# Kernel optimization log

Hardware: AMD Instinct MI355X
Metric: run time of the kernel (lower is better)

## Reference

```python
import jax, jax.numpy as jnp
import numpy as np


def ternarize_weight(w):
    # abs-mean threshold quantization to {-am, 0, +am}
    abs_mean = jnp.maximum(jnp.abs(w).mean(), 1e-5)
    thr = 0.7 * abs_mean
    q = jnp.where(w > thr, 1.0, jnp.where(w < -thr, -1.0, 0.0))
    # STE: forward value is q*abs_mean, grad flows to w as identity
    return w + jax.lax.stop_gradient(q * abs_mean - w)


def rotate_half(x):
    x1, x2 = jnp.split(x, 2, axis=-1)
    return jnp.concatenate([-x2, x1], axis=-1)


def setup_inputs() -> dict:
    key = jax.random.key(0)
    k1, k2, k3, k4, k5 = jax.random.split(key, 5)
    B, T, C, H = 2, 2048, 1024, 16
    D = C // H
    x = jax.random.normal(k1, (B, T, C), dtype=jnp.float32)
    cos = jax.random.uniform(k2, (1, 1, T, D), dtype=jnp.float32)
    sin = jax.random.uniform(k3, (1, 1, T, D), dtype=jnp.float32)
    w_qkv = jax.random.normal(k4, (3 * C, C), dtype=jnp.float32) / np.sqrt(C)
    w_proj = jax.random.normal(k5, (C, C), dtype=jnp.float32) / np.sqrt(C)
    return {"x": x, "cos": cos, "sin": sin, "w_qkv": w_qkv, "w_proj": w_proj}


def reference(x, cos, sin, w_qkv, w_proj):
    B, T, C = x.shape
    H = 16
    D = C // H
    wq = ternarize_weight(w_qkv)
    wp = ternarize_weight(w_proj)
    qkv = x @ wq.T  # [B,T,3C]
    q, k, v = jnp.split(qkv, 3, axis=-1)
    # [B,T,C] -> [B,H,T,D]
    q = q.reshape(B, T, H, D).transpose(0, 2, 1, 3)
    k = k.reshape(B, T, H, D).transpose(0, 2, 1, 3)
    v = v.reshape(B, T, H, D).transpose(0, 2, 1, 3)
    # RoPE
    q = q * cos + rotate_half(q) * sin
    k = k * cos + rotate_half(k) * sin
    # causal SDPA
    scale = 1.0 / np.sqrt(D)
    scores = jnp.einsum("bhqd,bhkd->bhqk", q, k) * scale
    causal = jnp.tril(jnp.ones((T, T), dtype=bool))
    scores = jnp.where(causal, scores, jnp.finfo(scores.dtype).min)
    attn = jax.nn.softmax(scores, axis=-1)
    y = jnp.einsum("bhqk,bhkd->bhqd", attn, v)  # [B,H,T,D]
    y = y.transpose(0, 2, 1, 3).reshape(B, T, C)
    return y @ wp.T
```

## Files before the change

kernel.cpp:

```cpp
#include <hip/hip_runtime.h>
#include <hip/hip_bf16.h>

#define B_ 2
#define T_ 2048
#define C_ 1024
#define H_ 16
#define D_ 64
#define M_ 4096
#define N3C 3072

using short8  = __attribute__((ext_vector_type(8))) short;
using floatx4 = __attribute__((ext_vector_type(4))) float;
typedef unsigned int u32;

__device__ __forceinline__ unsigned short f2b(float f) {
  __hip_bfloat16 h = __float2bfloat16(f);
  return *reinterpret_cast<unsigned short*>(&h);
}
__device__ __forceinline__ float b2f(unsigned short u) {
  union { unsigned int i; float f; } x; x.i = ((unsigned int)u) << 16; return x.f;
}

__device__ __forceinline__ void gll16(const void* g, void* l) {
  __builtin_amdgcn_global_load_lds((const __attribute__((address_space(1))) u32*)g,
                                   (__attribute__((address_space(3))) u32*)l, 16, 0, 0);
}


__global__ void zero_sums(double* sums) {
  if (threadIdx.x < 2) sums[threadIdx.x] = 0.0;
}

__global__ void abs_sum2(const float* __restrict__ wq, const float* __restrict__ wp,
                         double* __restrict__ sums) {
  __shared__ double red[4];
  const float* w = blockIdx.y ? wp : wq;
  const int n4 = blockIdx.y ? (C_ * C_ / 4) : (3 * C_ * C_ / 4);
  int stride = gridDim.x * blockDim.x;
  double s = 0.0;
  for (int i = blockIdx.x * blockDim.x + threadIdx.x; i < n4; i += stride) {
    float4 v = ((const float4*)w)[i];
    s += (double)fabsf(v.x) + (double)fabsf(v.y) + (double)fabsf(v.z) + (double)fabsf(v.w);
  }
  #pragma unroll
  for (int off = 32; off > 0; off >>= 1)
    s += __shfl_down(s, off, 64);
  if ((threadIdx.x & 63) == 0) red[threadIdx.x >> 6] = s;
  __syncthreads();
  if (threadIdx.x == 0) atomicAdd(sums + blockIdx.y, (red[0] + red[1]) + (red[2] + red[3]));
}

__global__ void ternarize_all(const float* __restrict__ wq, const float* __restrict__ wp,
                              unsigned short* __restrict__ oq, unsigned short* __restrict__ op,
                              const double* __restrict__ sums, float* __restrict__ ams) {
  const int NQ = 3 * C_ * C_;
  const int NP = C_ * C_;
  int i = blockIdx.x * blockDim.x + threadIdx.x;
  float am0 = fmaxf((float)(sums[0] * (1.0 / NQ)), 1e-5f);
  float am1 = fmaxf((float)(sums[1] * (1.0 / NP)), 1e-5f);
  if (i == 0) { ams[0] = am0; ams[1] = am1; }
  if (i < NQ) {
    float thr = 0.7f * am0, x = wq[i];
    oq[i] = (x > thr) ? 0x3F80u : ((x < -thr) ? 0xBF80u : 0u);
  } else if (i < NQ + NP) {
    int j = i - NQ;
    float thr = 0.7f * am1, x = wp[j];
    op[j] = (x > thr) ? 0x3F80u : ((x < -thr) ? 0xBF80u : 0u);
  }
}

__global__ void cvt_f32_bf16(const float* __restrict__ in, unsigned short* __restrict__ out, int n4) {
  int i = blockIdx.x * blockDim.x + threadIdx.x;
  if (i < n4) {
    float4 v = ((const float4*)in)[i];
    ushort4 o; o.x = f2b(v.x); o.y = f2b(v.y); o.z = f2b(v.z); o.w = f2b(v.w);
    ((ushort4*)out)[i] = o;
  }
}


__global__ __launch_bounds__(256) void gemm_qkv(const unsigned short* __restrict__ A,
                                                const unsigned short* __restrict__ W,
                                                const float* __restrict__ scale_ptr,
                                                const float* __restrict__ cosp,
                                                const float* __restrict__ sinp,
                                                unsigned short* __restrict__ Qb,
                                                unsigned short* __restrict__ Kb,
                                                unsigned short* __restrict__ Vb) {
  const int K = C_;
  __shared__ __attribute__((aligned(16))) unsigned short As[128 * 32];
  __shared__ __attribute__((aligned(16))) unsigned short Ws[128 * 32];
  const int tid = threadIdx.x, lane = tid & 63, wv = tid >> 6;
  const int m = lane & 15, g = lane >> 4;
  const int m0 = blockIdx.y * 128, n0 = blockIdx.x * 128;
  const int wm = (wv >> 1) * 64, wn = (wv & 1) * 64;

  const int srow = wv * 16 + (lane >> 2);
  const int skoff = (lane & 3) * 8;
  const unsigned short* ga0 = A + (size_t)(m0 + srow) * K + skoff;
  const unsigned short* ga1 = A + (size_t)(m0 + 64 + srow) * K + skoff;
  const unsigned short* gw0 = W + (size_t)(n0 + srow) * K + skoff;
  const unsigned short* gw1 = W + (size_t)(n0 + 64 + srow) * K + skoff;
  unsigned short* la0 = As + (wv * 16) * 32;
  unsigned short* la1 = As + (64 + wv * 16) * 32;
  unsigned short* lw0 = Ws + (wv * 16) * 32;
  unsigned short* lw1 = Ws + (64 + wv * 16) * 32;

  floatx4 acc[4][4] = {};
  for (int kc = 0; kc < K; kc += 32) {
    __syncthreads();
    gll16(ga0, la0); gll16(ga1, la1); gll16(gw0, lw0); gll16(gw1, lw1);
    ga0 += 32; ga1 += 32; gw0 += 32; gw1 += 32;
    __syncthreads();
    short8 af[4], wf[4];
    #pragma unroll
    for (int r = 0; r < 4; r++)
      af[r] = *(const short8*)&As[(wm + r * 16 + m) * 32 + g * 8];
    #pragma unroll
    for (int c = 0; c < 4; c++)
      wf[c] = *(const short8*)&Ws[(wn + c * 16 + m) * 32 + g * 8];
    #pragma unroll
    for (int r = 0; r < 4; r++)
      #pragma unroll
      for (int c = 0; c < 4; c++)
        acc[r][c] = __builtin_amdgcn_mfma_f32_16x16x32_bf16(af[r], wf[c], acc[r][c], 0, 0, 0);
  }

  const float am = *scale_ptr;
  const int sect = n0 >> 10;
  const int nloc = n0 & 1023;
  const int h = (nloc + wn) >> 6;
  if (sect < 2) {
    unsigned short* dst = sect ? Kb : Qb;
    const float sc = sect ? am : am * 0.18033688011112042f;
    #pragma unroll
    for (int r = 0; r < 4; r++)
      #pragma unroll
      for (int i = 0; i < 4; i++) {
        int row = m0 + wm + r * 16 + g * 4 + i;
        int t = row & (T_ - 1), b = row >> 11;
        size_t obase = ((size_t)(b * H_ + h) * T_ + t) * 64;
        #pragma unroll
        for (int c = 0; c < 4; c++) {
          int p = c * 16 + m;
          float cv = cosp[t * 64 + p], sv = sinp[t * 64 + p];
          float a = acc[r][c][i], pt = acc[r][c ^ 2][i];
          float val = (c < 2) ? (a * cv - pt * sv) : (a * cv + pt * sv);
          dst[obase + p] = f2b(val * sc);
        }
      }
  } else {
    #pragma unroll
    for (int r = 0; r < 4; r++)
      #pragma unroll
      for (int i = 0; i < 4; i++) {
        int row = m0 + wm + r * 16 + g * 4 + i;
        int t = row & (T_ - 1), b = row >> 11;
        size_t obase = ((size_t)(b * H_ + h) * T_ + t) * 64;
        #pragma unroll
        for (int c = 0; c < 4; c++)
          Vb[obase + c * 16 + m] = f2b(acc[r][c][i] * am);
      }
  }
}


__global__ __launch_bounds__(256) void gemm128(const unsigned short* __restrict__ A,
                                               const unsigned short* __restrict__ W,
                                               const float* __restrict__ scale_ptr,
                                               float* __restrict__ Cout,
                                               int N, int K) {
  __shared__ __attribute__((aligned(16))) unsigned short As[128 * 32];
  __shared__ __attribute__((aligned(16))) unsigned short Ws[128 * 32];
  const int tid = threadIdx.x, lane = tid & 63, wv = tid >> 6;
  const int m = lane & 15, g = lane >> 4;
  const int m0 = blockIdx.y * 128, n0 = blockIdx.x * 128;
  const int wm = (wv >> 1) * 64, wn = (wv & 1) * 64;

  const int srow = wv * 16 + (lane >> 2);
  const int skoff = (lane & 3) * 8;
  const unsigned short* ga0 = A + (size_t)(m0 + srow) * K + skoff;
  const unsigned short* ga1 = A + (size_t)(m0 + 64 + srow) * K + skoff;
  const unsigned short* gw0 = W + (size_t)(n0 + srow) * K + skoff;
  const unsigned short* gw1 = W + (size_t)(n0 + 64 + srow) * K + skoff;
  unsigned short* la0 = As + (wv * 16) * 32;
  unsigned short* la1 = As + (64 + wv * 16) * 32;
  unsigned short* lw0 = Ws + (wv * 16) * 32;
  unsigned short* lw1 = Ws + (64 + wv * 16) * 32;

  floatx4 acc[4][4] = {};
  for (int kc = 0; kc < K; kc += 32) {
    __syncthreads();
    gll16(ga0, la0); gll16(ga1, la1); gll16(gw0, lw0); gll16(gw1, lw1);
    ga0 += 32; ga1 += 32; gw0 += 32; gw1 += 32;
    __syncthreads();
    short8 af[4], wf[4];
    #pragma unroll
    for (int r = 0; r < 4; r++)
      af[r] = *(const short8*)&As[(wm + r * 16 + m) * 32 + g * 8];
    #pragma unroll
    for (int c = 0; c < 4; c++)
      wf[c] = *(const short8*)&Ws[(wn + c * 16 + m) * 32 + g * 8];
    #pragma unroll
    for (int r = 0; r < 4; r++)
      #pragma unroll
      for (int c = 0; c < 4; c++)
        acc[r][c] = __builtin_amdgcn_mfma_f32_16x16x32_bf16(af[r], wf[c], acc[r][c], 0, 0, 0);
  }

  const float scale = *scale_ptr;
  #pragma unroll
  for (int r = 0; r < 4; r++)
    #pragma unroll
    for (int c = 0; c < 4; c++)
      #pragma unroll
      for (int i = 0; i < 4; i++) {
        int row = m0 + wm + r * 16 + g * 4 + i;
        int col = n0 + wn + c * 16 + m;
        Cout[(size_t)row * N + col] = acc[r][c][i] * scale;
      }
}


__global__ __launch_bounds__(256) void v_transpose(const unsigned short* __restrict__ Vb,
                                                   unsigned short* __restrict__ Vtb) {
  __shared__ unsigned short L[64][65];
  const int bh = blockIdx.y, t0 = blockIdx.x * 64;
  const size_t hb = (size_t)bh * T_ * 64;
  #pragma unroll
  for (int it = 0; it < 16; it++) {
    int idx = it * 256 + threadIdx.x;
    int tl = idx >> 6, d = idx & 63;
    L[tl][d] = Vb[hb + (size_t)(t0 + tl) * 64 + d];
  }
  __syncthreads();
  #pragma unroll
  for (int it = 0; it < 16; it++) {
    int idx = it * 256 + threadIdx.x;
    int dr = idx >> 6, tl = idx & 63;
    Vtb[hb + (size_t)dr * T_ + t0 + tl] = L[tl][dr];
  }
}


__global__ __launch_bounds__(256) void flash_mfma(const unsigned short* __restrict__ Qb,
                                                  const unsigned short* __restrict__ Kb,
                                                  const unsigned short* __restrict__ Vtb,
                                                  unsigned short* __restrict__ Y) {
  __shared__ __align__(16) unsigned short Ktile[2][64][64];
  __shared__ __align__(16) unsigned short Vtile[2][64][64];
  __shared__ __align__(16) unsigned short Plds[4][16][72];
  const int lane = threadIdx.x & 63;
  const int wv = threadIdx.x >> 6;
  const int m = lane & 15, g = lane >> 4;
  const int gid = blockIdx.x;
  const int xcd = gid & 7, j = gid >> 3;
  const int bh = xcd * 4 + (j >> 4);
  const int pr = j & 15;
  const int b = bh >> 4, h = bh & 15;
  const size_t hb = (size_t)bh * T_ * 64;
  const unsigned short* Kbh = Kb + hb;
  const unsigned short* Vbh = Vtb + hb;
  const int r8 = lane >> 3, cc8 = lane & 7;
  const int gcol = ((cc8 ^ r8) << 3);

  #pragma unroll
  for (int sp = 0; sp < 2; sp++) {
    const int s = sp ? pr : (31 - pr);
    const int qbase = s * 64 + wv * 16;
    const int q_glob = qbase + m;
    const int ntiles = s + 1;

    const unsigned short* qp = Qb + hb + (size_t)(qbase + m) * 64 + g * 8;
    short8 qf0 = *(const short8*)qp;
    short8 qf1 = *(const short8*)(qp + 32);

    floatx4 O[4] = {};
    float lsum = 0.f;

    if (sp) __syncthreads();
    #pragma unroll
    for (int cc = 0; cc < 2; cc++) {
      int row = wv * 16 + cc * 8;
      gll16(Kbh + (size_t)(row + r8) * 64 + gcol, &Ktile[0][row][0]);
      gll16(Vbh + (size_t)(row + r8) * T_ + gcol, &Vtile[0][row][0]);
    }

    for (int kt = 0; kt < ntiles; kt++) {
      const int buf = kt & 1;
      const int kb = kt * 64;
      __syncthreads();
      if (kt + 1 < ntiles) {
        const int kb2 = kb + 64;
        #pragma unroll
        for (int cc = 0; cc < 2; cc++) {
          int row = wv * 16 + cc * 8;
          gll16(Kbh + (size_t)(kb2 + row + r8) * 64 + gcol, &Ktile[1 - buf][row][0]);
          gll16(Vbh + (size_t)(row + r8) * T_ + kb2 + gcol, &Vtile[1 - buf][row][0]);
        }
      }
      floatx4 S[4];
      #pragma unroll
      for (int mt = 0; mt < 4; mt++) {
        int row = mt * 16 + m;
        short8 kf0 = *(const short8*)&Ktile[buf][row][(g ^ (m & 7)) << 3];
        short8 kf1 = *(const short8*)&Ktile[buf][row][((g + 4) ^ (m & 7)) << 3];
        floatx4 sv = {};
        sv = __builtin_amdgcn_mfma_f32_16x16x32_bf16(kf0, qf0, sv, 0, 0, 0);
        sv = __builtin_amdgcn_mfma_f32_16x16x32_bf16(kf1, qf1, sv, 0, 0, 0);
        S[mt] = sv;
      }
      if (kt + 1 < ntiles) {
        #pragma unroll
        for (int mt = 0; mt < 4; mt++) {
          float e0 = exp2f(S[mt][0]), e1 = exp2f(S[mt][1]);
          float e2 = exp2f(S[mt][2]), e3 = exp2f(S[mt][3]);
          lsum += (e0 + e1) + (e2 + e3);
          ushort4 o; o.x = f2b(e0); o.y = f2b(e1); o.z = f2b(e2); o.w = f2b(e3);
          *(ushort4*)&Plds[wv][m][mt * 16 + g * 4] = o;
        }
      } else {
        #pragma unroll
        for (int mt = 0; mt < 4; mt++) {
          float e[4];
          #pragma unroll
          for (int r = 0; r < 4; r++) {
            int kg = kb + mt * 16 + g * 4 + r;
            e[r] = (kg <= q_glob) ? exp2f(S[mt][r]) : 0.f;
          }
          lsum += (e[0] + e[1]) + (e[2] + e[3]);
          ushort4 o; o.x = f2b(e[0]); o.y = f2b(e[1]); o.z = f2b(e[2]); o.w = f2b(e[3]);
          *(ushort4*)&Plds[wv][m][mt * 16 + g * 4] = o;
        }
      }
      short8 pa0 = *(const short8*)&Plds[wv][m][g * 8];
      short8 pa1 = *(const short8*)&Plds[wv][m][32 + g * 8];
      #pragma unroll
      for (int nt = 0; nt < 4; nt++) {
        int row = nt * 16 + m;
        short8 v0 = *(const short8*)&Vtile[buf][row][(g ^ (m & 7)) << 3];
        short8 v1 = *(const short8*)&Vtile[buf][row][((g + 4) ^ (m & 7)) << 3];
        O[nt] = __builtin_amdgcn_mfma_f32_16x16x32_bf16(pa0, v0, O[nt], 0, 0, 0);
        O[nt] = __builtin_amdgcn_mfma_f32_16x16x32_bf16(pa1, v1, O[nt], 0, 0, 0);
      }
    }

    lsum += __shfl_xor(lsum, 16, 64);
    lsum += __shfl_xor(lsum, 32, 64);
    float li[4];
    #pragma unroll
    for (int r = 0; r < 4; r++) li[r] = 1.0f / __shfl(lsum, g * 4 + r, 64);
    #pragma unroll
    for (int nt = 0; nt < 4; nt++)
      #pragma unroll
      for (int r = 0; r < 4; r++) {
        int trow = qbase + g * 4 + r;
        int col = h * 64 + nt * 16 + m;
        Y[(size_t)(b * T_ + trow) * C_ + col] = f2b(O[nt][r] * li[r]);
      }
  }
}


extern "C" void kernel_launch(void* const* d_in, const int* in_sizes, int n_in,
                              void* d_out, int out_size, void* d_ws, size_t ws_size,
                              hipStream_t stream) {
  (void)in_sizes; (void)n_in; (void)out_size; (void)ws_size;
  const float* x      = (const float*)d_in[0];
  const float* cosp   = (const float*)d_in[1];
  const float* sinp   = (const float*)d_in[2];
  const float* w_qkv  = (const float*)d_in[3];
  const float* w_proj = (const float*)d_in[4];
  float* out = (float*)d_out;

  char* ws = (char*)d_ws;
  double* sums = (double*)ws;
  float*  ams  = (float*)(ws + 16);
  unsigned short* wqkv_b  = (unsigned short*)(ws + 256);
  unsigned short* wproj_b = wqkv_b + (size_t)N3C * C_;
  unsigned short* xb      = wproj_b + (size_t)C_ * C_;
  unsigned short* Qb      = xb + (size_t)M_ * C_;
  unsigned short* Kb      = Qb + (size_t)B_ * H_ * T_ * D_;
  unsigned short* Vb      = Kb + (size_t)B_ * H_ * T_ * D_;
  unsigned short* Vtb     = Vb + (size_t)B_ * H_ * T_ * D_;
  unsigned short* yb      = Vtb + (size_t)B_ * H_ * T_ * D_;

  zero_sums<<<1, 64, 0, stream>>>(sums);
  abs_sum2<<<dim3(256, 2), 256, 0, stream>>>(w_qkv, w_proj, sums);
  ternarize_all<<<(4 * C_ * C_) / 256, 256, 0, stream>>>(w_qkv, w_proj, wqkv_b, wproj_b,
                                                         sums, ams);
  cvt_f32_bf16<<<(M_ * C_ / 4 + 255) / 256, 256, 0, stream>>>(x, xb, M_ * C_ / 4);
  gemm_qkv<<<dim3(N3C / 128, M_ / 128), 256, 0, stream>>>(xb, wqkv_b, ams + 0,
                                                          cosp, sinp, Qb, Kb, Vb);
  v_transpose<<<dim3(T_ / 64, B_ * H_), 256, 0, stream>>>(Vb, Vtb);
  flash_mfma<<<512, 256, 0, stream>>>(Qb, Kb, Vtb, yb);
  gemm128<<<dim3(C_ / 128, M_ / 128), 256, 0, stream>>>(yb, wproj_b, ams + 1, out, C_, C_);
}
```

Before: 225.5 us.

## Fuse weight/activation conversion, write V transposed, widen flash query tiles

```diff
diff --git a/kernel.cpp b/kernel.cpp
--- a/kernel.cpp
+++ b/kernel.cpp
@@ -26,10 +26,6 @@
                                    (__attribute__((address_space(3))) u32*)l, 16, 0, 0);
 }
 
-
-__global__ void zero_sums(double* sums) {
-  if (threadIdx.x < 2) sums[threadIdx.x] = 0.0;
-}
 
 __global__ void abs_sum2(const float* __restrict__ wq, const float* __restrict__ wp,
                          double* __restrict__ sums) {
@@ -50,9 +46,11 @@
   if (threadIdx.x == 0) atomicAdd(sums + blockIdx.y, (red[0] + red[1]) + (red[2] + red[3]));
 }
 
-__global__ void ternarize_all(const float* __restrict__ wq, const float* __restrict__ wp,
-                              unsigned short* __restrict__ oq, unsigned short* __restrict__ op,
-                              const double* __restrict__ sums, float* __restrict__ ams) {
+__global__ void tern_cvt(const float* __restrict__ wq, const float* __restrict__ wp,
+                         const float* __restrict__ x,
+                         unsigned short* __restrict__ oq, unsigned short* __restrict__ op,
+                         unsigned short* __restrict__ xb,
+                         const double* __restrict__ sums, float* __restrict__ ams) {
   const int NQ = 3 * C_ * C_;
   const int NP = C_ * C_;
   int i = blockIdx.x * blockDim.x + threadIdx.x;
@@ -60,21 +58,17 @@
   float am1 = fmaxf((float)(sums[1] * (1.0 / NP)), 1e-5f);
   if (i == 0) { ams[0] = am0; ams[1] = am1; }
   if (i < NQ) {
-    float thr = 0.7f * am0, x = wq[i];
-    oq[i] = (x > thr) ? 0x3F80u : ((x < -thr) ? 0xBF80u : 0u);
+    float thr = 0.7f * am0, v = wq[i];
+    oq[i] = (v > thr) ? 0x3F80u : ((v < -thr) ? 0xBF80u : 0u);
   } else if (i < NQ + NP) {
     int j = i - NQ;
-    float thr = 0.7f * am1, x = wp[j];
-    op[j] = (x > thr) ? 0x3F80u : ((x < -thr) ? 0xBF80u : 0u);
-  }
-}
-
-__global__ void cvt_f32_bf16(const float* __restrict__ in, unsigned short* __restrict__ out, int n4) {
-  int i = blockIdx.x * blockDim.x + threadIdx.x;
-  if (i < n4) {
-    float4 v = ((const float4*)in)[i];
+    float thr = 0.7f * am1, v = wp[j];
+    op[j] = (v > thr) ? 0x3F80u : ((v < -thr) ? 0xBF80u : 0u);
+  } else {
+    int j = i - NQ - NP;
+    float4 v = ((const float4*)x)[j];
     ushort4 o; o.x = f2b(v.x); o.y = f2b(v.y); o.z = f2b(v.z); o.w = f2b(v.w);
-    ((ushort4*)out)[i] = o;
+    ((ushort4*)xb)[j] = o;
   }
 }
 
@@ -86,7 +80,7 @@
                                                 const float* __restrict__ sinp,
                                                 unsigned short* __restrict__ Qb,
                                                 unsigned short* __restrict__ Kb,
-                                                unsigned short* __restrict__ Vb) {
+                                                unsigned short* __restrict__ Vtb) {
   const int K = C_;
   __shared__ __attribute__((aligned(16))) unsigned short As[128 * 32];
   __shared__ __attribute__((aligned(16))) unsigned short Ws[128 * 32];
@@ -156,10 +150,10 @@
       for (int i = 0; i < 4; i++) {
         int row = m0 + wm + r * 16 + g * 4 + i;
         int t = row & (T_ - 1), b = row >> 11;
-        size_t obase = ((size_t)(b * H_ + h) * T_ + t) * 64;
+        size_t hbase = (size_t)(b * H_ + h) * 64 * T_;
         #pragma unroll
         for (int c = 0; c < 4; c++)
-          Vb[obase + c * 16 + m] = f2b(acc[r][c][i] * am);
+          Vtb[hbase + (size_t)(c * 16 + m) * T_ + t] = f2b(acc[r][c][i] * am);
       }
   }
 }
@@ -219,27 +213,6 @@
         int col = n0 + wn + c * 16 + m;
         Cout[(size_t)row * N + col] = acc[r][c][i] * scale;
       }
-}
-
-
-__global__ __launch_bounds__(256) void v_transpose(const unsigned short* __restrict__ Vb,
-                                                   unsigned short* __restrict__ Vtb) {
-  __shared__ unsigned short L[64][65];
-  const int bh = blockIdx.y, t0 = blockIdx.x * 64;
-  const size_t hb = (size_t)bh * T_ * 64;
-  #pragma unroll
-  for (int it = 0; it < 16; it++) {
-    int idx = it * 256 + threadIdx.x;
-    int tl = idx >> 6, d = idx & 63;
-    L[tl][d] = Vb[hb + (size_t)(t0 + tl) * 64 + d];
-  }
-  __syncthreads();
-  #pragma unroll
-  for (int it = 0; it < 16; it++) {
-    int idx = it * 256 + threadIdx.x;
-    int dr = idx >> 6, tl = idx & 63;
-    Vtb[hb + (size_t)dr * T_ + t0 + tl] = L[tl][dr];
-  }
 }
 
 
@@ -255,8 +228,8 @@
   const int m = lane & 15, g = lane >> 4;
   const int gid = blockIdx.x;
   const int xcd = gid & 7, j = gid >> 3;
-  const int bh = xcd * 4 + (j >> 4);
-  const int pr = j & 15;
+  const int bh = xcd * 4 + (j & 3);
+  const int s = 15 - (j >> 2);
   const int b = bh >> 4, h = bh & 15;
   const size_t hb = (size_t)bh * T_ * 64;
   const unsigned short* Kbh = Kb + hb;
@@ -264,41 +237,43 @@
   const int r8 = lane >> 3, cc8 = lane & 7;
   const int gcol = ((cc8 ^ r8) << 3);
 
+  const int ntiles = 2 * s + 2;
+  const int qb0 = s * 128 + wv * 32;
+  const int qb1 = qb0 + 16;
+
+  const unsigned short* qp0 = Qb + hb + (size_t)(qb0 + m) * 64 + g * 8;
+  short8 qf00 = *(const short8*)qp0;
+  short8 qf01 = *(const short8*)(qp0 + 32);
+  const unsigned short* qp1 = qp0 + 16 * 64;
+  short8 qf10 = *(const short8*)qp1;
+  short8 qf11 = *(const short8*)(qp1 + 32);
+
+  floatx4 O0[4] = {}, O1[4] = {};
+  float ls0 = 0.f, ls1 = 0.f;
+
   #pragma unroll
-  for (int sp = 0; sp < 2; sp++) {
-    const int s = sp ? pr : (31 - pr);
-    const int qbase = s * 64 + wv * 16;
-    const int q_glob = qbase + m;
-    const int ntiles = s + 1;
-
-    const unsigned short* qp = Qb + hb + (size_t)(qbase + m) * 64 + g * 8;
-    short8 qf0 = *(const short8*)qp;
-    short8 qf1 = *(const short8*)(qp + 32);
-
-    floatx4 O[4] = {};
-    float lsum = 0.f;
-
-    if (sp) __syncthreads();
-    #pragma unroll
-    for (int cc = 0; cc < 2; cc++) {
-      int row = wv * 16 + cc * 8;
-      gll16(Kbh + (size_t)(row + r8) * 64 + gcol, &Ktile[0][row][0]);
-      gll16(Vbh + (size_t)(row + r8) * T_ + gcol, &Vtile[0][row][0]);
+  for (int cc = 0; cc < 2; cc++) {
+    int row = wv * 16 + cc * 8;
+    gll16(Kbh + (size_t)(row + r8) * 64 + gcol, &Ktile[0][row][0]);
+    gll16(Vbh + (size_t)(row + r8) * T_ + gcol, &Vtile[0][row][0]);
+  }
+
+  for (int kt = 0; kt < ntiles; kt++) {
+    const int buf = kt & 1;
+    const int kb = kt * 64;
+    __syncthreads();
+    if (kt + 1 < ntiles) {
+      const int kb2 = kb + 64;
+      #pragma unroll
+      for (int cc = 0; cc < 2; cc++) {
+        int row = wv * 16 + cc * 8;
+        gll16(Kbh + (size_t)(kb2 + row + r8) * 64 + gcol, &Ktile[1 - buf][row][0]);
+        gll16(Vbh + (size_t)(row + r8) * T_ + kb2 + gcol, &Vtile[1 - buf][row][0]);
+      }
     }
-
-    for (int kt = 0; kt < ntiles; kt++) {
-      const int buf = kt & 1;
-      const int kb = kt * 64;
-      __syncthreads();
-      if (kt + 1 < ntiles) {
-        const int kb2 = kb + 64;
-        #pragma unroll
-        for (int cc = 0; cc < 2; cc++) {
-          int row = wv * 16 + cc * 8;
-          gll16(Kbh + (size_t)(kb2 + row + r8) * 64 + gcol, &Ktile[1 - buf][row][0]);
-          gll16(Vbh + (size_t)(row + r8) * T_ + kb2 + gcol, &Vtile[1 - buf][row][0]);
-        }
-      }
+    if (kb > qb0 + 31) continue;
+
+    auto do_qset = [&](short8 qa, short8 qb_, int qbase, float& lsum, floatx4* O) {
       floatx4 S[4];
       #pragma unroll
       for (int mt = 0; mt < 4; mt++) {
@@ -306,11 +281,11 @@
         short8 kf0 = *(const short8*)&Ktile[buf][row][(g ^ (m & 7)) << 3];
         short8 kf1 = *(const short8*)&Ktile[buf][row][((g + 4) ^ (m & 7)) << 3];
         floatx4 sv = {};
-        sv = __builtin_amdgcn_mfma_f32_16x16x32_bf16(kf0, qf0, sv, 0, 0, 0);
-        sv = __builtin_amdgcn_mfma_f32_16x16x32_bf16(kf1, qf1, sv, 0, 0, 0);
+        sv = __builtin_amdgcn_mfma_f32_16x16x32_bf16(kf0, qa, sv, 0, 0, 0);
+        sv = __builtin_amdgcn_mfma_f32_16x16x32_bf16(kf1, qb_, sv, 0, 0, 0);
         S[mt] = sv;
       }
-      if (kt + 1 < ntiles) {
+      if (kb + 64 <= qbase) {
         #pragma unroll
         for (int mt = 0; mt < 4; mt++) {
           float e0 = exp2f(S[mt][0]), e1 = exp2f(S[mt][1]);
@@ -320,6 +295,7 @@
           *(ushort4*)&Plds[wv][m][mt * 16 + g * 4] = o;
         }
       } else {
+        const int q_glob = qbase + m;
         #pragma unroll
         for (int mt = 0; mt < 4; mt++) {
           float e[4];
@@ -343,8 +319,17 @@
         O[nt] = __builtin_amdgcn_mfma_f32_16x16x32_bf16(pa0, v0, O[nt], 0, 0, 0);
         O[nt] = __builtin_amdgcn_mfma_f32_16x16x32_bf16(pa1, v1, O[nt], 0, 0, 0);
       }
-    }
-
+    };
+
+    do_qset(qf00, qf01, qb0, ls0, O0);
+    if (kb <= qb1 + 15) do_qset(qf10, qf11, qb1, ls1, O1);
+  }
+
+  #pragma unroll
+  for (int jq = 0; jq < 2; jq++) {
+    float lsum = jq ? ls1 : ls0;
+    floatx4* O = jq ? O1 : O0;
+    const int qbase = jq ? qb1 : qb0;
     lsum += __shfl_xor(lsum, 16, 64);
     lsum += __shfl_xor(lsum, 32, 64);
     float li[4];
@@ -381,18 +366,16 @@
   unsigned short* xb      = wproj_b + (size_t)C_ * C_;
   unsigned short* Qb      = xb + (size_t)M_ * C_;
   unsigned short* Kb      = Qb + (size_t)B_ * H_ * T_ * D_;
-  unsigned short* Vb      = Kb + (size_t)B_ * H_ * T_ * D_;
-  unsigned short* Vtb     = Vb + (size_t)B_ * H_ * T_ * D_;
+  unsigned short* Vtb     = Kb + (size_t)B_ * H_ * T_ * D_;
   unsigned short* yb      = Vtb + (size_t)B_ * H_ * T_ * D_;
 
-  zero_sums<<<1, 64, 0, stream>>>(sums);
+  hipMemsetAsync(sums, 0, 16, stream);
   abs_sum2<<<dim3(256, 2), 256, 0, stream>>>(w_qkv, w_proj, sums);
-  ternarize_all<<<(4 * C_ * C_) / 256, 256, 0, stream>>>(w_qkv, w_proj, wqkv_b, wproj_b,
-                                                         sums, ams);
-  cvt_f32_bf16<<<(M_ * C_ / 4 + 255) / 256, 256, 0, stream>>>(x, xb, M_ * C_ / 4);
+  tern_cvt<<<(4 * C_ * C_ + M_ * C_ / 4) / 256, 256, 0, stream>>>(w_qkv, w_proj, x,
+                                                                  wqkv_b, wproj_b, xb,
+                                                                  sums, ams);
   gemm_qkv<<<dim3(N3C / 128, M_ / 128), 256, 0, stream>>>(xb, wqkv_b, ams + 0,
-                                                          cosp, sinp, Qb, Kb, Vb);
-  v_transpose<<<dim3(T_ / 64, B_ * H_), 256, 0, stream>>>(Vb, Vtb);
+                                                          cosp, sinp, Qb, Kb, Vtb);
   flash_mfma<<<512, 256, 0, stream>>>(Qb, Kb, Vtb, yb);
   gemm128<<<dim3(C_ / 128, M_ / 128), 256, 0, stream>>>(yb, wproj_b, ams + 1, out, C_, C_);
 }
```

Measured after the change: 227.1 us. No clear change (+0.7%).
